# Performance work log

Hardware: AMD Instinct MI355X
Metric: run time of the kernel (lower is better)

Reference implementation:

```python
import jax, jax.numpy as jnp
import numpy as np

X_MIN, X_MAX = -3.0, 3.0
EPS = 1e-08


def setup_inputs() -> dict:
    key = jax.random.key(0)
    k1, k2, k3 = jax.random.split(key, 3)
    B, D_in, D_out, K = 8192, 512, 128, 16
    x = jax.random.normal(k1, (B, D_in), dtype=jnp.float32)
    # trunc_normal_(std=0.02) approximated by scaled normal
    weights = jax.random.normal(k2, (D_out, D_in, K), dtype=jnp.float32) * 0.02
    # xavier_uniform for skip
    limit = float(np.sqrt(6.0 / (D_in + D_out)))
    skip_w = jax.random.uniform(k3, (D_out, D_in), dtype=jnp.float32,
                                minval=-limit, maxval=limit)
    bias = jnp.zeros((D_out,), dtype=jnp.float32)
    return {"x": x, "weights": weights, "skip_w": skip_w, "bias": bias}


def reference(x, weights, skip_w, bias):
    # x: (B, D_in); weights: (D_out, D_in, K); skip_w: (D_out, D_in); bias: (D_out,)
    K = weights.shape[-1]
    t = jnp.clip((x - X_MIN) / (X_MAX - X_MIN + EPS), 0.0, 1.0)
    pos = t * (K - 1)
    idx0 = jnp.floor(pos).astype(jnp.int32)
    idx1 = jnp.minimum(idx0 + 1, K - 1)
    frac = jnp.clip(pos - idx0.astype(pos.dtype), 0.0, 1.0)
    # Hat-basis coefficients per (b, i): avoids materializing (B, D_out, D_in)
    oh0 = jax.nn.one_hot(idx0, K, dtype=x.dtype)  # (B, D_in, K)
    oh1 = jax.nn.one_hot(idx1, K, dtype=x.dtype)
    c = oh0 * (1.0 - frac)[..., None] + oh1 * frac[..., None]  # (B, D_in, K)
    # y[b,o] = sum_i (1-frac)*w[o,i,idx0] + frac*w[o,i,idx1]
    y = jnp.einsum('bik,oik->bo', c, weights)
    y = y + bias + x @ skip_w.T
    return y
```

## Files before the change

kernel.cpp:

```cpp
#include <hip/hip_runtime.h>

typedef __attribute__((ext_vector_type(8))) short short8;
typedef __attribute__((ext_vector_type(4))) float f32x4;

#define DIN 512
#define DOUT 128
#define KK 16
#define BTOT 8192
#define KAUG (DIN * KK + DIN)
#define NCHUNK_TOT (KAUG / 128)
#define NSPL 4
#define CPB (NCHUNK_TOT / NSPL)
#define BM 64
#define CHUNK_BYTES 32768
#define CBASE 32768
#define LDS_BYTES 49152

__device__ static inline unsigned short f2bf(float x) {
  unsigned u = __builtin_bit_cast(unsigned, x);
  return (unsigned short)((u + 0x7FFFu + ((u >> 16) & 1u)) >> 16);
}

__device__ static inline void llds16(const char* g, char* l) {
  __builtin_amdgcn_global_load_lds(
      (const __attribute__((address_space(1))) unsigned int*)g,
      (__attribute__((address_space(3))) unsigned int*)l, 16, 0, 0);
}

__global__ __launch_bounds__(256) void build_wpp(const float* __restrict__ w,
                                                 const float* __restrict__ sk,
                                                 unsigned short* __restrict__ wpp) {
  const int gi = blockIdx.x * 256 + threadIdx.x;
  const int g = gi >> 11;
  const int rem = gi & 2047;
  const int o = rem >> 4;
  const int kcs = rem & 15;
  const int kc = kcs ^ (o & 15);
  const int kglob = g * 128 + kc * 8;
  const float* src = (kglob < 8192) ? (w + (size_t)o * 8192 + kglob)
                                    : (sk + (size_t)o * 512 + (kglob - 8192));
  const float4 v0 = ((const float4*)src)[0];
  const float4 v1 = ((const float4*)src)[1];
  uint4 pk;
  pk.x = f2bf(v0.x) | ((unsigned)f2bf(v0.y) << 16);
  pk.y = f2bf(v0.z) | ((unsigned)f2bf(v0.w) << 16);
  pk.z = f2bf(v1.x) | ((unsigned)f2bf(v1.y) << 16);
  pk.w = f2bf(v1.z) | ((unsigned)f2bf(v1.w) << 16);
  ((uint4*)wpp)[gi] = pk;
}

__global__ __launch_bounds__(256, 2) void kan_mfma(const float* __restrict__ x,
                                                   const unsigned short* __restrict__ wpp,
                                                   const float* __restrict__ bias,
                                                   float* __restrict__ out) {
  __shared__ __align__(16) char smem[LDS_BYTES];
  const int tid = threadIdx.x;
  const int bt = blockIdx.x >> 2;
  const int sp = blockIdx.x & 3;
  const int b0 = bt * BM;
  const int wid = tid >> 6, lane = tid & 63;
  const int lr = lane & 15, lq = lane >> 4;
  const int wm = wid & 1, wn = wid >> 1;

  f32x4 acc[2][4] = {};

  for (int c = 0; c < CPB; ++c) {
    const int g = sp * CPB + c;
    __syncthreads();

    {
      const char* gsrc = ((const char*)wpp) + (size_t)g * CHUNK_BYTES + wid * 8192 + lane * 16;
      char* ldst = smem + wid * 8192;
#pragma unroll
      for (int it = 0; it < 8; ++it)
        llds16(gsrc + it * 1024, ldst + it * 1024);
    }

    if (g < 64) {
      const int ibase = g * 8;
#pragma unroll
      for (int hh = 0; hh < 2; ++hh) {
        const int p = tid + hh * 256;
        const int bl = p >> 3, il = p & 7;
        const float xv = x[(size_t)(b0 + bl) * DIN + ibase + il];
        float t = fminf(fmaxf((xv + 3.0f) * (1.0f / 6.0f), 0.0f), 1.0f);
        const float pos = t * 15.0f;
        int i0 = (int)pos;
        i0 = i0 > 14 ? 14 : i0;
        const float f = pos - (float)i0;
        char* row = smem + CBASE + bl * 256;
        const int swz = bl & 15;
        char* g0 = row + (((il * 2) ^ swz) << 4);
        char* g1 = row + (((il * 2 + 1) ^ swz) << 4);
        *(uint4*)g0 = make_uint4(0, 0, 0, 0);
        *(uint4*)g1 = make_uint4(0, 0, 0, 0);
        const unsigned short h0 = f2bf(1.0f - f);
        const unsigned short h1 = f2bf(f);
        const int i1 = i0 + 1;
        *(unsigned short*)(((i0 & 8) ? g1 : g0) + (i0 & 7) * 2) = h0;
        *(unsigned short*)(((i1 & 8) ? g1 : g0) + (i1 & 7) * 2) = h1;
      }
    } else {
      const int ioff = (g - 64) * 128;
      const int bl = tid >> 2, q = tid & 3;
      const float* xr = x + (size_t)(b0 + bl) * DIN + ioff;
      char* row = smem + CBASE + bl * 256;
      const int swz = bl & 15;
#pragma unroll
      for (int gg = 0; gg < 4; ++gg) {
        const int kc = q * 4 + gg;
        const float4 v0 = ((const float4*)(xr + kc * 8))[0];
        const float4 v1 = ((const float4*)(xr + kc * 8))[1];
        uint4 pk;
        pk.x = f2bf(v0.x) | ((unsigned)f2bf(v0.y) << 16);
        pk.y = f2bf(v0.z) | ((unsigned)f2bf(v0.w) << 16);
        pk.z = f2bf(v1.x) | ((unsigned)f2bf(v1.y) << 16);
        pk.w = f2bf(v1.z) | ((unsigned)f2bf(v1.w) << 16);
        *(uint4*)(row + ((kc ^ swz) << 4)) = pk;
      }
    }
    __syncthreads();

#pragma unroll
    for (int ks = 0; ks < 4; ++ks) {
      const int swq = ((ks * 4 + lq) ^ lr) << 4;
      short8 af[2], bfr[4];
#pragma unroll
      for (int mt = 0; mt < 2; ++mt) {
        const int m = wm * 32 + mt * 16 + lr;
        af[mt] = *(const short8*)(smem + CBASE + m * 256 + swq);
      }
#pragma unroll
      for (int nt = 0; nt < 4; ++nt) {
        const int o = wn * 64 + nt * 16 + lr;
        bfr[nt] = *(const short8*)(smem + o * 256 + swq);
      }
#pragma unroll
      for (int mt = 0; mt < 2; ++mt)
#pragma unroll
        for (int nt = 0; nt < 4; ++nt)
          acc[mt][nt] = __builtin_amdgcn_mfma_f32_16x16x32_bf16(af[mt], bfr[nt], acc[mt][nt], 0, 0, 0);
    }
  }

#pragma unroll
  for (int nt = 0; nt < 4; ++nt) {
    const int col = wn * 64 + nt * 16 + lr;
    const float bv = (sp == 0) ? bias[col] : 0.0f;
#pragma unroll
    for (int mt = 0; mt < 2; ++mt) {
      const int rowb = b0 + wm * 32 + mt * 16 + lq * 4;
#pragma unroll
      for (int r = 0; r < 4; ++r)
        atomicAdd(out + (size_t)(rowb + r) * DOUT + col, acc[mt][nt][r] + bv);
    }
  }
}

__global__ void kan_naive(const float* __restrict__ x, const float* __restrict__ w,
                          const float* __restrict__ skw, const float* __restrict__ bias,
                          float* __restrict__ out) {
  const int b = blockIdx.x;
  const int o = threadIdx.x;
  float acc = bias[o];
  for (int i = 0; i < DIN; ++i) {
    float xv = x[(size_t)b * DIN + i];
    float t = fminf(fmaxf((xv + 3.0f) * (1.0f / 6.0f), 0.0f), 1.0f);
    float p = t * 15.0f;
    float fi = floorf(p);
    int i0 = (int)fi;
    int i1 = (i0 < 15) ? i0 + 1 : 15;
    float f = p - fi;
    const float* wr = &w[((size_t)o * DIN + i) * KK];
    acc += (1.0f - f) * wr[i0] + f * wr[i1] + xv * skw[(size_t)o * DIN + i];
  }
  out[(size_t)b * DOUT + o] = acc;
}

extern "C" void kernel_launch(void* const* d_in, const int* in_sizes, int n_in,
                              void* d_out, int out_size, void* d_ws, size_t ws_size,
                              hipStream_t stream) {
  const float* x    = (const float*)d_in[0];
  const float* w    = (const float*)d_in[1];
  const float* skw  = (const float*)d_in[2];
  const float* bias = (const float*)d_in[3];
  float* out = (float*)d_out;

  const size_t need = (size_t)NCHUNK_TOT * CHUNK_BYTES;
  if (ws_size < need) {
    kan_naive<<<BTOT, DOUT, 0, stream>>>(x, w, skw, bias, out);
    return;
  }

  unsigned short* wpp = (unsigned short*)d_ws;

  hipMemsetAsync(d_out, 0, (size_t)out_size * sizeof(float), stream);
  build_wpp<<<NCHUNK_TOT * 2048 / 256, 256, 0, stream>>>(w, skw, wpp);
  kan_mfma<<<(BTOT / BM) * NSPL, 256, 0, stream>>>(x, wpp, bias, out);
}
```

Before: 109.4 us.

## Switch to fp16 MFMA with transposed x, k-major LDS layout, larger tiles

Moves the matmul from bf16 to fp16 MFMA and adds a kernel that writes an fp16 transposed copy of x, so each lane reads contiguous batch elements when building the hat basis. The hat coefficients are computed as a vectorised max(1-|pos-k|,0) over 16 lanes in half precision. LDS moves from a swizzled row-major layout to a k-major slab layout, the batch tile grows to 128 with a 4x4 accumulator per wave, and the K split goes from 4 to 8 with chunks interleaved. The cost is an extra transpose pass, a larger LDS footprint, and fp16 range and precision risk, including the hat positions being rounded to fp16.

```diff
diff --git a/kernel.cpp b/kernel.cpp
--- a/kernel.cpp
+++ b/kernel.cpp
@@ -1,25 +1,18 @@
 #include <hip/hip_runtime.h>
 
-typedef __attribute__((ext_vector_type(8))) short short8;
-typedef __attribute__((ext_vector_type(4))) float f32x4;
+typedef _Float16 half8 __attribute__((ext_vector_type(8)));
+typedef _Float16 h16 __attribute__((ext_vector_type(16)));
+typedef float f32x4 __attribute__((ext_vector_type(4)));
 
 #define DIN 512
 #define DOUT 128
-#define KK 16
 #define BTOT 8192
-#define KAUG (DIN * KK + DIN)
-#define NCHUNK_TOT (KAUG / 128)
-#define NSPL 4
-#define CPB (NCHUNK_TOT / NSPL)
-#define BM 64
+#define NCHUNK 68
+#define NSPL 8
+#define BM 128
 #define CHUNK_BYTES 32768
 #define CBASE 32768
-#define LDS_BYTES 49152
-
-__device__ static inline unsigned short f2bf(float x) {
-  unsigned u = __builtin_bit_cast(unsigned, x);
-  return (unsigned short)((u + 0x7FFFu + ((u >> 16) & 1u)) >> 16);
-}
+#define LDS_BYTES 65536
 
 __device__ static inline void llds16(const char* g, char* l) {
   __builtin_amdgcn_global_load_lds(
@@ -27,119 +20,147 @@
       (__attribute__((address_space(3))) unsigned int*)l, 16, 0, 0);
 }
 
+__device__ static inline unsigned short f2h(float x) {
+  _Float16 h = (_Float16)x;
+  return __builtin_bit_cast(unsigned short, h);
+}
+
 __global__ __launch_bounds__(256) void build_wpp(const float* __restrict__ w,
                                                  const float* __restrict__ sk,
                                                  unsigned short* __restrict__ wpp) {
-  const int gi = blockIdx.x * 256 + threadIdx.x;
-  const int g = gi >> 11;
-  const int rem = gi & 2047;
-  const int o = rem >> 4;
-  const int kcs = rem & 15;
-  const int kc = kcs ^ (o & 15);
-  const int kglob = g * 128 + kc * 8;
+  const int gid = blockIdx.x * 256 + threadIdx.x;
+  const int g = gid >> 11;
+  const int rem = gid & 2047;
+  const int p = rem >> 7;
+  const int o = rem & 127;
+  const int kglob = g * 128 + p * 8;
   const float* src = (kglob < 8192) ? (w + (size_t)o * 8192 + kglob)
                                     : (sk + (size_t)o * 512 + (kglob - 8192));
   const float4 v0 = ((const float4*)src)[0];
   const float4 v1 = ((const float4*)src)[1];
   uint4 pk;
-  pk.x = f2bf(v0.x) | ((unsigned)f2bf(v0.y) << 16);
-  pk.y = f2bf(v0.z) | ((unsigned)f2bf(v0.w) << 16);
-  pk.z = f2bf(v1.x) | ((unsigned)f2bf(v1.y) << 16);
-  pk.w = f2bf(v1.z) | ((unsigned)f2bf(v1.w) << 16);
-  ((uint4*)wpp)[gi] = pk;
-}
-
-__global__ __launch_bounds__(256, 2) void kan_mfma(const float* __restrict__ x,
-                                                   const unsigned short* __restrict__ wpp,
-                                                   const float* __restrict__ bias,
-                                                   float* __restrict__ out) {
+  pk.x = f2h(v0.x) | ((unsigned)f2h(v0.y) << 16);
+  pk.y = f2h(v0.z) | ((unsigned)f2h(v0.w) << 16);
+  pk.z = f2h(v1.x) | ((unsigned)f2h(v1.y) << 16);
+  pk.w = f2h(v1.z) | ((unsigned)f2h(v1.w) << 16);
+  ((uint4*)wpp)[gid] = pk;
+}
+
+__global__ __launch_bounds__(256) void xpose(const float* __restrict__ x,
+                                             _Float16* __restrict__ xt) {
+  __shared__ _Float16 t[32][33];
+  const int c0 = blockIdx.x * 32;
+  const int r0 = blockIdx.y * 32;
+  const int tx = threadIdx.x & 31, ty = threadIdx.x >> 5;
+#pragma unroll
+  for (int j = 0; j < 32; j += 8)
+    t[ty + j][tx] = (_Float16)x[(size_t)(r0 + ty + j) * DIN + c0 + tx];
+  __syncthreads();
+#pragma unroll
+  for (int j = 0; j < 32; j += 8)
+    xt[(size_t)(c0 + ty + j) * BTOT + r0 + tx] = t[tx][ty + j];
+}
+
+__global__ __launch_bounds__(256, 2) void kan_mfma(
+    const float* __restrict__ x, const _Float16* __restrict__ xt,
+    const unsigned short* __restrict__ wpp, const float* __restrict__ bias,
+    float* __restrict__ out) {
   __shared__ __align__(16) char smem[LDS_BYTES];
   const int tid = threadIdx.x;
-  const int bt = blockIdx.x >> 2;
-  const int sp = blockIdx.x & 3;
+  const int bt = blockIdx.x >> 3;
+  const int sp = blockIdx.x & 7;
   const int b0 = bt * BM;
   const int wid = tid >> 6, lane = tid & 63;
   const int lr = lane & 15, lq = lane >> 4;
   const int wm = wid & 1, wn = wid >> 1;
 
-  f32x4 acc[2][4] = {};
-
-  for (int c = 0; c < CPB; ++c) {
-    const int g = sp * CPB + c;
+  const h16 iota16 = {(_Float16)0, (_Float16)1, (_Float16)2, (_Float16)3,
+                      (_Float16)4, (_Float16)5, (_Float16)6, (_Float16)7,
+                      (_Float16)8, (_Float16)9, (_Float16)10, (_Float16)11,
+                      (_Float16)12, (_Float16)13, (_Float16)14, (_Float16)15};
+  const h16 one16 = {(_Float16)1, (_Float16)1, (_Float16)1, (_Float16)1,
+                     (_Float16)1, (_Float16)1, (_Float16)1, (_Float16)1,
+                     (_Float16)1, (_Float16)1, (_Float16)1, (_Float16)1,
+                     (_Float16)1, (_Float16)1, (_Float16)1, (_Float16)1};
+  const h16 zero16 = {};
+
+  f32x4 acc[4][4] = {};
+
+  for (int c = 0; c < 9; ++c) {
+    int g;
+    bool skipc;
+    if (c < 8) { g = sp + c * 8; skipc = false; }
+    else { if (sp >= 4) break; g = 64 + sp; skipc = true; }
+
     __syncthreads();
 
     {
-      const char* gsrc = ((const char*)wpp) + (size_t)g * CHUNK_BYTES + wid * 8192 + lane * 16;
+      const char* gsrc = (const char*)wpp + (size_t)g * CHUNK_BYTES + wid * 8192 + lane * 16;
       char* ldst = smem + wid * 8192;
 #pragma unroll
       for (int it = 0; it < 8; ++it)
         llds16(gsrc + it * 1024, ldst + it * 1024);
     }
 
-    if (g < 64) {
-      const int ibase = g * 8;
+    if (!skipc) {
+      const int ib = g * 8;
 #pragma unroll
       for (int hh = 0; hh < 2; ++hh) {
-        const int p = tid + hh * 256;
-        const int bl = p >> 3, il = p & 7;
-        const float xv = x[(size_t)(b0 + bl) * DIN + ibase + il];
-        float t = fminf(fmaxf((xv + 3.0f) * (1.0f / 6.0f), 0.0f), 1.0f);
-        const float pos = t * 15.0f;
-        int i0 = (int)pos;
-        i0 = i0 > 14 ? 14 : i0;
-        const float f = pos - (float)i0;
-        char* row = smem + CBASE + bl * 256;
-        const int swz = bl & 15;
-        char* g0 = row + (((il * 2) ^ swz) << 4);
-        char* g1 = row + (((il * 2 + 1) ^ swz) << 4);
-        *(uint4*)g0 = make_uint4(0, 0, 0, 0);
-        *(uint4*)g1 = make_uint4(0, 0, 0, 0);
-        const unsigned short h0 = f2bf(1.0f - f);
-        const unsigned short h1 = f2bf(f);
-        const int i1 = i0 + 1;
-        *(unsigned short*)(((i0 & 8) ? g1 : g0) + (i0 & 7) * 2) = h0;
-        *(unsigned short*)(((i1 & 8) ? g1 : g0) + (i1 & 7) * 2) = h1;
+        const int il = wid * 2 + hh;
+#pragma unroll
+        for (int rh = 0; rh < 2; ++rh) {
+          const int r = lane + rh * 64;
+          const float xv = (float)xt[(size_t)(ib + il) * BTOT + b0 + r];
+          float t = fminf(fmaxf((xv + 3.0f) * (1.0f / 6.0f), 0.0f), 1.0f);
+          const float pos = t * 15.0f;
+          const _Float16 ph = (_Float16)pos;
+          h16 pv;
+#pragma unroll
+          for (int q = 0; q < 16; ++q) pv[q] = ph;
+          h16 d = __builtin_elementwise_abs(pv - iota16);
+          h16 cc = __builtin_elementwise_max(one16 - d, zero16);
+          char* base = smem + CBASE + (2 * il) * 2048 + r * 16;
+          *(uint4*)base = ((const uint4*)&cc)[0];
+          *(uint4*)(base + 2048) = ((const uint4*)&cc)[1];
+        }
       }
     } else {
       const int ioff = (g - 64) * 128;
-      const int bl = tid >> 2, q = tid & 3;
-      const float* xr = x + (size_t)(b0 + bl) * DIN + ioff;
-      char* row = smem + CBASE + bl * 256;
-      const int swz = bl & 15;
-#pragma unroll
-      for (int gg = 0; gg < 4; ++gg) {
-        const int kc = q * 4 + gg;
-        const float4 v0 = ((const float4*)(xr + kc * 8))[0];
-        const float4 v1 = ((const float4*)(xr + kc * 8))[1];
-        uint4 pk;
-        pk.x = f2bf(v0.x) | ((unsigned)f2bf(v0.y) << 16);
-        pk.y = f2bf(v0.z) | ((unsigned)f2bf(v0.w) << 16);
-        pk.z = f2bf(v1.x) | ((unsigned)f2bf(v1.y) << 16);
-        pk.w = f2bf(v1.z) | ((unsigned)f2bf(v1.w) << 16);
-        *(uint4*)(row + ((kc ^ swz) << 4)) = pk;
+#pragma unroll
+      for (int pp = 0; pp < 4; ++pp) {
+        const int p = wid * 4 + pp;
+#pragma unroll
+        for (int rh = 0; rh < 2; ++rh) {
+          const int r = lane + rh * 64;
+          const float* src = x + (size_t)(b0 + r) * DIN + ioff + p * 8;
+          const float4 v0 = ((const float4*)src)[0];
+          const float4 v1 = ((const float4*)src)[1];
+          uint4 pk;
+          pk.x = f2h(v0.x) | ((unsigned)f2h(v0.y) << 16);
+          pk.y = f2h(v0.z) | ((unsigned)f2h(v0.w) << 16);
+          pk.z = f2h(v1.x) | ((unsigned)f2h(v1.y) << 16);
+          pk.w = f2h(v1.z) | ((unsigned)f2h(v1.w) << 16);
+          *(uint4*)(smem + CBASE + p * 2048 + r * 16) = pk;
+        }
       }
     }
     __syncthreads();
 
 #pragma unroll
     for (int ks = 0; ks < 4; ++ks) {
-      const int swq = ((ks * 4 + lq) ^ lr) << 4;
-      short8 af[2], bfr[4];
-#pragma unroll
-      for (int mt = 0; mt < 2; ++mt) {
-        const int m = wm * 32 + mt * 16 + lr;
-        af[mt] = *(const short8*)(smem + CBASE + m * 256 + swq);
-      }
-#pragma unroll
-      for (int nt = 0; nt < 4; ++nt) {
-        const int o = wn * 64 + nt * 16 + lr;
-        bfr[nt] = *(const short8*)(smem + o * 256 + swq);
-      }
-#pragma unroll
-      for (int mt = 0; mt < 2; ++mt)
+      const int slab = (ks * 4 + lq) * 2048 + lr * 16;
+      half8 af[4], bf[4];
+#pragma unroll
+      for (int mt = 0; mt < 4; ++mt)
+        af[mt] = *(const half8*)(smem + CBASE + slab + (wm * 64 + mt * 16) * 16);
+#pragma unroll
+      for (int nt = 0; nt < 4; ++nt)
+        bf[nt] = *(const half8*)(smem + slab + (wn * 64 + nt * 16) * 16);
+#pragma unroll
+      for (int mt = 0; mt < 4; ++mt)
 #pragma unroll
         for (int nt = 0; nt < 4; ++nt)
-          acc[mt][nt] = __builtin_amdgcn_mfma_f32_16x16x32_bf16(af[mt], bfr[nt], acc[mt][nt], 0, 0, 0);
+          acc[mt][nt] = __builtin_amdgcn_mfma_f32_16x16x32_f16(af[mt], bf[nt], acc[mt][nt], 0, 0, 0);
     }
   }
 
@@ -148,11 +169,11 @@
     const int col = wn * 64 + nt * 16 + lr;
     const float bv = (sp == 0) ? bias[col] : 0.0f;
 #pragma unroll
-    for (int mt = 0; mt < 2; ++mt) {
-      const int rowb = b0 + wm * 32 + mt * 16 + lq * 4;
+    for (int mt = 0; mt < 4; ++mt) {
+      const int row0 = b0 + wm * 64 + mt * 16 + lq * 4;
 #pragma unroll
       for (int r = 0; r < 4; ++r)
-        atomicAdd(out + (size_t)(rowb + r) * DOUT + col, acc[mt][nt][r] + bv);
+        atomicAdd(out + (size_t)(row0 + r) * DOUT + col, acc[mt][nt][r] + bv);
     }
   }
 }
@@ -171,7 +192,7 @@
     int i0 = (int)fi;
     int i1 = (i0 < 15) ? i0 + 1 : 15;
     float f = p - fi;
-    const float* wr = &w[((size_t)o * DIN + i) * KK];
+    const float* wr = &w[((size_t)o * DIN + i) * 16];
     acc += (1.0f - f) * wr[i0] + f * wr[i1] + xv * skw[(size_t)o * DIN + i];
   }
   out[(size_t)b * DOUT + o] = acc;
@@ -186,15 +207,18 @@
   const float* bias = (const float*)d_in[3];
   float* out = (float*)d_out;
 
-  const size_t need = (size_t)NCHUNK_TOT * CHUNK_BYTES;
-  if (ws_size < need) {
+  const size_t xt_bytes = (size_t)DIN * BTOT * sizeof(_Float16);
+  const size_t wpp_bytes = (size_t)NCHUNK * CHUNK_BYTES;
+  if (ws_size < xt_bytes + wpp_bytes) {
     kan_naive<<<BTOT, DOUT, 0, stream>>>(x, w, skw, bias, out);
     return;
   }
 
-  unsigned short* wpp = (unsigned short*)d_ws;
-
-  hipMemsetAsync(d_out, 0, (size_t)out_size * sizeof(float), stream);
-  build_wpp<<<NCHUNK_TOT * 2048 / 256, 256, 0, stream>>>(w, skw, wpp);
-  kan_mfma<<<(BTOT / BM) * NSPL, 256, 0, stream>>>(x, wpp, bias, out);
-}
+  _Float16* xt = (_Float16*)d_ws;
+  unsigned short* wpp = (unsigned short*)((char*)d_ws + xt_bytes);
+
+  (void)hipMemsetAsync(d_out, 0, (size_t)out_size * sizeof(float), stream);
+  build_wpp<<<NCHUNK * 2048 / 256, 256, 0, stream>>>(w, skw, wpp);
+  xpose<<<dim3(DIN / 32, BTOT / 32), 256, 0, stream>>>(x, xt);
+  kan_mfma<<<(BTOT / BM) * NSPL, 256, 0, stream>>>(x, xt, wpp, bias, out);
+}
```

Result: slower. 122.5 us (+12.0%).
